# Optimization experiments

Hardware: AMD Instinct MI355X
Metric: run time of the kernel (lower is better)

Reference implementation:

```python
import jax, jax.numpy as jnp
import numpy as np

B, S, IN, IN2, H = 512, 256, 300, 300, 512
FN = 3  # filter_num


def setup_inputs() -> dict:
    key = jax.random.key(0)
    ks = jax.random.split(key, 16)
    def n(k, shape, scale=0.05):
        return jax.random.normal(k, shape, dtype=jnp.float32) * scale
    return {
        "x": jax.random.normal(ks[0], (B, S, IN), dtype=jnp.float32),
        "W_in": n(ks[1], (IN, IN2)), "b_in": n(ks[2], (IN2,)),
        "Wih": n(ks[3], (IN2, 4 * H)), "Whh": n(ks[4], (H, 4 * H)),
        "bih": n(ks[5], (4 * H,)), "bhh": n(ks[6], (4 * H,)),
        "Q": n(ks[7], (H, IN2)), "R": n(ks[8], (IN2, H)),
        "Wc3": n(ks[9], (FN, 1, 3, H)), "bc3": n(ks[10], (FN,)),
        "Wc4": n(ks[11], (FN, 1, 4, H)), "bc4": n(ks[12], (FN,)),
        "Wc5": n(ks[13], (FN, 1, 5, H)), "bc5": n(ks[14], (FN,)),
        "W_lin": n(ks[15], (3 * FN, 2)), "b_lin": jnp.zeros((2,), jnp.float32),
    }


def reference(x, W_in, b_in, Wih, Whh, bih, bhh, Q, R,
              Wc3, bc3, Wc4, bc4, Wc5, bc5, W_lin, b_lin):
    # input projection: [B,S,IN] -> [B,S,IN2]
    xin = jnp.tanh(x @ W_in + b_in)
    xs = jnp.swapaxes(xin, 0, 1)  # [S,B,IN2] for scan
    bsz = x.shape[0]
    h0 = jnp.zeros((bsz, H), x.dtype)
    c0 = jnp.zeros((bsz, H), x.dtype)

    def step(carry, xt):
        ht, Ct = carry
        # mogrify, mog_iterations=2: i=1 odd updates x, i=2 even updates h
        xt = 2.0 * jax.nn.sigmoid(ht @ Q) * xt
        ht = 2.0 * jax.nn.sigmoid(xt @ R) * ht
        gates = xt @ Wih + bih + ht @ Whh + bhh  # [B,4H]
        i, f, g, o = jnp.split(gates, 4, axis=1)
        Ct = jax.nn.sigmoid(f) * Ct + jax.nn.sigmoid(i) * jnp.tanh(g)
        ht = jax.nn.sigmoid(o) * jnp.tanh(Ct)
        return (ht, Ct), ht

    _, hs = jax.lax.scan(step, (h0, c0), xs)  # [S,B,H]
    hmap = jnp.swapaxes(hs, 0, 1)[:, None, :, :]  # [B,1,S,H]

    feats = []
    for w, b in ((Wc3, bc3), (Wc4, bc4), (Wc5, bc5)):
        y = jax.lax.conv_general_dilated(
            hmap, w, (1, 1), 'VALID',
            dimension_numbers=('NCHW', 'OIHW', 'NCHW'))
        y = jax.nn.relu(y + b[None, :, None, None])  # [B,FN,S-fsz+1,1]
        feats.append(jnp.max(y, axis=(2, 3)))  # global max pool -> [B,FN]
    cat = jnp.concatenate(feats, axis=1)  # [B, 3*FN]
    # dropout is identity at inference
    return cat @ W_lin + b_lin  # [B,2]
```

## Files before the change

kernel.cpp:

```cpp
#include <hip/hip_runtime.h>

#define DI __device__ __forceinline__

typedef __attribute__((ext_vector_type(4))) float  f32x4;
typedef __attribute__((ext_vector_type(8))) short  s16x8;
typedef __attribute__((ext_vector_type(8))) __bf16 bf16x8;
typedef unsigned long long u64;

constexpr int S_   = 256;
constexpr int B_   = 512;
constexpr int KP_  = 320;
constexpr int ALD_ = 832;
constexpr int NRING = 34;
constexpr int NWG  = 512;
constexpr size_t HSLOT = 512 * 512;

constexpr size_t OFF_XIN = 0;
constexpr size_t SZ_XIN  = (size_t)S_ * B_ * KP_ * 2;
constexpr size_t OFF_U   = OFF_XIN + SZ_XIN;
constexpr size_t SZ_U    = (size_t)B_ * S_ * 64 * 4;
constexpr size_t OFF_HS  = OFF_U + SZ_U;
constexpr size_t SZ_HS   = (size_t)NRING * HSLOT * 2;
constexpr size_t OFF_ACT = OFF_HS + SZ_HS;
constexpr size_t SZ_ACT  = (size_t)B_ * ALD_ * 2;
constexpr size_t OFF_WPT = OFF_ACT + SZ_ACT;
constexpr size_t SZ_WPT  = (size_t)320 * 320 * 2;
constexpr size_t OFF_QPT = OFF_WPT + SZ_WPT;
constexpr size_t SZ_QPT  = (size_t)320 * 512 * 2;
constexpr size_t OFF_RPT = OFF_QPT + SZ_QPT;
constexpr size_t SZ_RPT  = (size_t)512 * 320 * 2;
constexpr size_t OFF_WGT = OFF_RPT + SZ_RPT;
constexpr size_t SZ_WGT  = (size_t)2048 * 832 * 2;
constexpr size_t OFF_BG  = OFF_WGT + SZ_WGT;
constexpr size_t SZ_BG   = 2048 * 4;
constexpr size_t OFF_VT  = OFF_BG + SZ_BG;
constexpr size_t SZ_VT   = (size_t)64 * 512 * 2;
constexpr size_t OFF_BAR = OFF_VT + SZ_VT;
constexpr size_t SZ_BAR  = 8192;
constexpr size_t WS_NEED = OFF_BAR + SZ_BAR;

DI unsigned short f2bf(float x) {
  unsigned int u = __float_as_uint(x);
  unsigned int r = (u + 0x7FFFu + ((u >> 16) & 1u)) >> 16;
  return (unsigned short)r;
}
DI float bf2f(unsigned short h) { return __uint_as_float(((unsigned int)h) << 16); }

DI float sigm(float x) {
  float e = __builtin_amdgcn_exp2f(x * -1.44269504088896f);
  return __builtin_amdgcn_rcpf(1.0f + e);
}
DI float tanh_(float x) {
  x = fminf(fmaxf(x, -15.0f), 15.0f);
  float e = __builtin_amdgcn_exp2f(x * 2.88539008177793f);
  return (e - 1.0f) * __builtin_amdgcn_rcpf(e + 1.0f);
}
DI bf16x8 asbf(s16x8 v) { return __builtin_bit_cast(bf16x8, v); }

DI u64 ld_sys_u64(const void* p) {
  return __hip_atomic_load((const u64*)p, __ATOMIC_RELAXED, __HIP_MEMORY_SCOPE_SYSTEM);
}
DI void st_sys_u64(void* p, u64 v) {
  __hip_atomic_store((u64*)p, v, __ATOMIC_RELAXED, __HIP_MEMORY_SCOPE_SYSTEM);
}
template<int N> DI void wait_vm() {
  asm volatile("s_waitcnt vmcnt(%0)" :: "n"(N) : "memory");
}

template<int NK>
DI void gemm2(const unsigned short* Ab, int lda,
              const unsigned short* Bb, int ldb,
              short* sA, short* sB, f32x4 acc[2])
{
  constexpr int NR = (NK + 1) / 2;
  const int tid  = threadIdx.x;
  const int tm   = tid >> 8;
  const int t8   = tid & 255;
  const int lane = tid & 63;
  const int l15  = lane & 15;
  const int kseg = (lane >> 4) * 8;
  const int w    = (tid >> 6) & 3;
  const int wm = w >> 1, wn = w & 1;
  const int sArow = t8 >> 3, sAcol = (t8 & 7) * 4;
  const int sBrow = t8 >> 2, sBcol = (t8 & 3) * 8;
  const unsigned short* gA = Ab + sArow * lda + sAcol;
  const unsigned short* gB = Bb + sBrow * ldb + sBcol;
  short* tA = sA + tm * 2048;
  short* tB = sB + tm * 4096;
  const int aoff = sArow * 32 + sAcol;
  const int boff = sBrow * 32 + sBcol;
  const int afr  = (wm * 16 + l15) * 32 + kseg;

  u64 a0, a1 = 0, b00, b01, b10 = 0, b11 = 0;
  a0  = ld_sys_u64(gA + tm * 32);
  b00 = ((const u64*)(gB + tm * 32))[0];
  b01 = ((const u64*)(gB + tm * 32))[1];
  if (2 + tm < NK) {
    a1  = ld_sys_u64(gA + (2 + tm) * 32);
    b10 = ((const u64*)(gB + (2 + tm) * 32))[0];
    b11 = ((const u64*)(gB + (2 + tm) * 32))[1];
  }
  *(u64*)&tA[aoff] = a0;
  *(u64*)&tB[boff] = b00; *(u64*)&tB[boff + 4] = b01;
  __syncthreads();
  #pragma unroll
  for (int j = 0; j < NR; ++j) {
    const int curA = (j & 1) * 1024, curB = (j & 1) * 2048;
    if (j + 2 < NR) {
      const int kt = (j + 2) * 2 + tm;
      if (kt < NK) {
        if ((j & 1) == 0) { a0 = ld_sys_u64(gA + kt * 32);
                            b00 = ((const u64*)(gB + kt * 32))[0];
                            b01 = ((const u64*)(gB + kt * 32))[1]; }
        else              { a1 = ld_sys_u64(gA + kt * 32);
                            b10 = ((const u64*)(gB + kt * 32))[0];
                            b11 = ((const u64*)(gB + kt * 32))[1]; }
      }
    }
    if (j * 2 + tm < NK) {
      s16x8 Af = *(const s16x8*)&tA[curA + afr];
      #pragma unroll
      for (int ni = 0; ni < 2; ++ni) {
        s16x8 Bf = *(const s16x8*)&tB[curB + (wn * 32 + ni * 16 + l15) * 32 + kseg];
        acc[ni] = __builtin_amdgcn_mfma_f32_16x16x32_bf16(asbf(Af), asbf(Bf), acc[ni], 0, 0, 0);
      }
    }
    if (j + 1 < NR) {
      const int kt = (j + 1) * 2 + tm;
      const int nxtA = ((j + 1) & 1) * 1024, nxtB = ((j + 1) & 1) * 2048;
      if (kt < NK) {
        if ((j & 1) == 0) { *(u64*)&tA[nxtA + aoff] = a1;
                            *(u64*)&tB[nxtB + boff] = b10; *(u64*)&tB[nxtB + boff + 4] = b11; }
        else              { *(u64*)&tA[nxtA + aoff] = a0;
                            *(u64*)&tB[nxtB + boff] = b00; *(u64*)&tB[nxtB + boff + 4] = b01; }
      }
    }
    __syncthreads();
  }
}

DI void reduce2(f32x4 acc[2], float* rbuf) {
  const int tid = threadIdx.x, t8 = tid & 255;
  if (tid >= 256) {
    #pragma unroll
    for (int ni = 0; ni < 2; ++ni)
      #pragma unroll
      for (int r = 0; r < 4; ++r)
        rbuf[(ni * 4 + r) * 256 + t8] = acc[ni][r];
  }
  __syncthreads();
  if (tid < 256) {
    #pragma unroll
    for (int ni = 0; ni < 2; ++ni)
      #pragma unroll
      for (int r = 0; r < 4; ++r)
        acc[ni][r] += rbuf[(ni * 4 + r) * 256 + t8];
  }
}

template<typename F>
DI void epiloop32(f32x4 acc[2], F&& f) {
  const int lane = threadIdx.x & 63;
  const int w = (threadIdx.x >> 6) & 3, wm = w >> 1, wn = w & 1;
  #pragma unroll
  for (int ni = 0; ni < 2; ++ni)
    #pragma unroll
    for (int r = 0; r < 4; ++r)
      f(wm * 16 + (lane >> 4) * 4 + r, wn * 32 + ni * 16 + (lane & 15), acc[ni][r]);
}

DI void pack_store32(const unsigned short* lds16, unsigned short* dstbase, int ldd) {
  const u64* l64 = (const u64*)lds16;
  const int i = threadIdx.x;
  const int row = i >> 4, q = i & 15;
  st_sys_u64(dstbase + row * ldd + q * 4, l64[i]);
}

template<int NK, int KREAL>
DI void gemm_f32A(const float* Af, int lda,
                  const unsigned short* Bb, int ldb,
                  short* sA, short* sB, f32x4 acc[2][2])
{
  const int tid  = threadIdx.x;
  const int lane = tid & 63;
  const int w = tid >> 6, wm = w >> 1, wn = w & 1;
  const float* ga = Af + (tid >> 2) * lda;
  const int cseg  = (tid & 3) * 8;
  const unsigned short* gb = Bb + (tid >> 2) * ldb + (tid & 3) * 8;
  const int arow0 = (wm * 32 + (lane & 15)) * 32 + (lane >> 4) * 8;
  const int brow0 = (wn * 32 + (lane & 15)) * 32 + (lane >> 4) * 8;

  auto loadA = [&](int k) -> s16x8 {
    s16x8 r;
    const int c0 = k * 32 + cseg;
    if (c0 + 8 <= KREAL) {
      float4 f0 = *(const float4*)(ga + c0);
      float4 f1 = *(const float4*)(ga + c0 + 4);
      r[0] = (short)f2bf(f0.x); r[1] = (short)f2bf(f0.y);
      r[2] = (short)f2bf(f0.z); r[3] = (short)f2bf(f0.w);
      r[4] = (short)f2bf(f1.x); r[5] = (short)f2bf(f1.y);
      r[6] = (short)f2bf(f1.z); r[7] = (short)f2bf(f1.w);
    } else {
      #pragma unroll
      for (int j = 0; j < 8; ++j) {
        float x = (c0 + j < KREAL) ? ga[c0 + j] : 0.0f;
        r[j] = (short)f2bf(x);
      }
    }
    return r;
  };

  s16x8 va = loadA(0);
  s16x8 vb = *(const s16x8*)gb;
  *(s16x8*)&sA[tid * 8] = va;
  *(s16x8*)&sB[tid * 8] = vb;
  __syncthreads();
  for (int k = 0; k < NK; ++k) {
    const int cur = (k & 1) * 2048;
    if (k + 1 < NK) {
      va = loadA(k + 1);
      vb = *(const s16x8*)(gb + (k + 1) * 32);
    }
    s16x8 a0 = *(const s16x8*)&sA[cur + arow0];
    s16x8 a1 = *(const s16x8*)&sA[cur + arow0 + 16 * 32];
    s16x8 b0 = *(const s16x8*)&sB[cur + brow0];
    s16x8 b1 = *(const s16x8*)&sB[cur + brow0 + 16 * 32];
    acc[0][0] = __builtin_amdgcn_mfma_f32_16x16x32_bf16(asbf(a0), asbf(b0), acc[0][0], 0, 0, 0);
    acc[0][1] = __builtin_amdgcn_mfma_f32_16x16x32_bf16(asbf(a0), asbf(b1), acc[0][1], 0, 0, 0);
    acc[1][0] = __builtin_amdgcn_mfma_f32_16x16x32_bf16(asbf(a1), asbf(b0), acc[1][0], 0, 0, 0);
    acc[1][1] = __builtin_amdgcn_mfma_f32_16x16x32_bf16(asbf(a1), asbf(b1), acc[1][1], 0, 0, 0);
    if (k + 1 < NK) {
      const int nxt = ((k + 1) & 1) * 2048;
      *(s16x8*)&sA[nxt + tid * 8] = va;
      *(s16x8*)&sB[nxt + tid * 8] = vb;
    }
    __syncthreads();
  }
}

template<typename F>
DI void epiloop(f32x4 acc[2][2], F&& f) {
  const int lane = threadIdx.x & 63;
  const int w = (threadIdx.x & 255) >> 6, wm = w >> 1, wn = w & 1;
  #pragma unroll
  for (int mi = 0; mi < 2; ++mi)
    #pragma unroll
    for (int ni = 0; ni < 2; ++ni)
      #pragma unroll
      for (int r = 0; r < 4; ++r) {
        const int rowl = wm * 32 + mi * 16 + (lane >> 4) * 4 + r;
        const int coll = wn * 32 + ni * 16 + (lane & 15);
        f(rowl, coll, acc[mi][ni][r]);
      }
}

__global__ void k_prep_wpt(const float* __restrict__ Wi, unsigned short* __restrict__ WpT) {
  int i = blockIdx.x * 256 + threadIdx.x;
  if (i >= 320 * 320) return;
  int n = i / 320, k = i % 320;
  float v = (n < 300 && k < 300) ? Wi[k * 300 + n] : 0.0f;
  WpT[i] = f2bf(v);
}
__global__ void k_prep_qpt(const float* __restrict__ Q, unsigned short* __restrict__ QpT) {
  int i = blockIdx.x * 256 + threadIdx.x;
  if (i >= 320 * 512) return;
  int n = i >> 9, k = i & 511;
  float v = (n < 300) ? Q[k * 300 + n] : 0.0f;
  QpT[i] = f2bf(v);
}
__global__ void k_prep_rpt(const float* __restrict__ R, unsigned short* __restrict__ RpT) {
  int i = blockIdx.x * 256 + threadIdx.x;
  if (i >= 512 * 320) return;
  int n = i / 320, k = i % 320;
  float v = (k < 300) ? R[k * 512 + n] : 0.0f;
  RpT[i] = f2bf(v);
}
__global__ void k_prep_wgt(const float* __restrict__ Wih, const float* __restrict__ Whh,
                           unsigned short* __restrict__ WgT) {
  int i = blockIdx.x * 256 + threadIdx.x;
  if (i >= 2048 * 832) return;
  int np = i / 832, k = i % 832;
  int c = np >> 2, g = np & 3, col = g * 512 + c;
  float v = 0.0f;
  if (k < 300) v = Wih[k * 2048 + col];
  else if (k >= 320) v = Whh[(k - 320) * 2048 + col];
  WgT[i] = f2bf(v);
}
__global__ void k_prep_bg(const float* __restrict__ bih, const float* __restrict__ bhh,
                          float* __restrict__ bg) {
  int i = blockIdx.x * 256 + threadIdx.x;
  if (i >= 2048) return;
  int c = i >> 2, g = i & 3, col = g * 512 + c;
  bg[i] = bih[col] + bhh[col];
}
__global__ void k_prep_vt(const float* __restrict__ Wc3, const float* __restrict__ Wc4,
                          const float* __restrict__ Wc5, unsigned short* __restrict__ VT) {
  int i = blockIdx.x * 256 + threadIdx.x;
  if (i >= 64 * 512) return;
  int j = i >> 9, k = i & 511;
  float v = 0.0f;
  if (j < 9)       { int f = j / 3,  dt = j % 3;        v = Wc3[(f * 3 + dt) * 512 + k]; }
  else if (j < 21) { int jj = j - 9;  int f = jj / 4, dt = jj % 4; v = Wc4[(f * 4 + dt) * 512 + k]; }
  else if (j < 36) { int jj = j - 21; int f = jj / 5, dt = jj % 5; v = Wc5[(f * 5 + dt) * 512 + k]; }
  VT[i] = f2bf(v);
}
__global__ void k_wsfail(float* out, int n, float v) {
  int i = blockIdx.x * 256 + threadIdx.x;
  if (i < n) out[i] = -v;
}

__global__ __launch_bounds__(256) void k_proj(const float* __restrict__ x,
                                              const unsigned short* __restrict__ WpT,
                                              const float* __restrict__ b_in,
                                              unsigned short* __restrict__ xin) {
  __shared__ short sA[4096], sB[4096];
  const int m0 = blockIdx.x * 64, n0 = blockIdx.y * 64;
  f32x4 acc[2][2];
  const f32x4 z = {0.f, 0.f, 0.f, 0.f};
  acc[0][0] = z; acc[0][1] = z; acc[1][0] = z; acc[1][1] = z;
  gemm_f32A<10, 300>(x + (size_t)m0 * 300, 300, WpT + n0 * 320, 320, sA, sB, acc);
  epiloop(acc, [&](int rowl, int coll, float vacc) {
    const int row = m0 + rowl, col = n0 + coll;
    float o = 0.0f;
    if (col < 300) o = tanh_(vacc + b_in[col]);
    const int b = row >> 8, s = row & 255;
    xin[(size_t)(s * 512 + b) * KP_ + col] = f2bf(o);
  });
}

__global__ __launch_bounds__(512, 4) void k_scan(
    const unsigned short* __restrict__ xin,
    const unsigned short* __restrict__ QpT,
    const unsigned short* __restrict__ RpT,
    const unsigned short* __restrict__ WgT,
    const float* __restrict__ bg,
    const unsigned short* __restrict__ VT,
    unsigned short* __restrict__ hs,
    unsigned short* __restrict__ act,
    float* __restrict__ U,
    unsigned int* __restrict__ bar)
{
  __shared__ short sA[4096];
  __shared__ short sB[8192];
  __shared__ float rbuf[2048];
  __shared__ float gbuf[2048];
  __shared__ unsigned short pbuf[2048];
  __shared__ unsigned short obuf[2048];
  const int wg   = blockIdx.x;
  const int grp  = wg >> 5;
  const int l    = wg & 31;
  const int tid  = threadIdx.x;
  const f32x4 z = {0.f, 0.f, 0.f, 0.f};

  const int gm0 = grp * 32;
  const int gn0 = l * 64;
  float c_state = 0.f;
  const int crow = tid >> 4, ccl = tid & 15;
  const float4 cb = *(const float4*)&bg[gn0 + ccl * 4];

  int ep = 0;
  auto bar_sync = [&]() {
    wait_vm<0>();
    __syncthreads();
    if (tid == 0) {
      __hip_atomic_fetch_add(&bar[grp * 64], 1u,
                             __ATOMIC_RELAXED, __HIP_MEMORY_SCOPE_AGENT);
      const unsigned tgt = (unsigned)(ep + 1) * 32u;
      while (__hip_atomic_load(&bar[grp * 64], __ATOMIC_RELAXED,
                               __HIP_MEMORY_SCOPE_AGENT) < tgt)
        __builtin_amdgcn_s_sleep(1);
    }
    __syncthreads();
    ++ep;
  };

  for (int t = 0; t < S_; ++t) {
    const unsigned short* hst = hs + (size_t)(t % NRING) * HSLOT;
    unsigned short*       hso = hs + (size_t)((t + 1) % NRING) * HSLOT;

    if (l < 5) {
      const int n0 = l * 64;
      {
        const unsigned short* xin_t = xin + ((size_t)t * 512 + gm0) * KP_;
        const int row = tid >> 4, q = tid & 15;
        ((u64*)pbuf)[tid] = *(const u64*)(xin_t + row * KP_ + n0 + q * 4);
      }
      f32x4 acc[2] = {z, z};
      gemm2<16>(hst + gm0 * 512, 512, QpT + n0 * 512, 512, sA, sB, acc);
      reduce2(acc, rbuf);
      if (tid < 256) {
        epiloop32(acc, [&](int row, int col, float v) {
          obuf[row * 64 + col] = f2bf(2.0f * sigm(v) * bf2f(pbuf[row * 64 + col]));
        });
      }
      __syncthreads();
      pack_store32(obuf, act + gm0 * ALD_ + n0, ALD_);
    }
    bar_sync();

    if (l < 8) {
      const int n0 = l * 64;
      {
        const int row = tid >> 4, q = tid & 15;
        ((u64*)pbuf)[tid] = ld_sys_u64(hst + (gm0 + row) * 512 + n0 + q * 4);
      }
      f32x4 acc[2] = {z, z};
      gemm2<10>(act + gm0 * ALD_, ALD_, RpT + n0 * KP_, KP_, sA, sB, acc);
      reduce2(acc, rbuf);
      if (tid < 256) {
        epiloop32(acc, [&](int row, int col, float v) {
          obuf[row * 64 + col] = f2bf(2.0f * sigm(v) * bf2f(pbuf[row * 64 + col]));
        });
      }
      __syncthreads();
      pack_store32(obuf, act + gm0 * ALD_ + 320 + n0, ALD_);
    }
    bar_sync();

    {
      f32x4 acc[2] = {z, z};
      gemm2<26>(act + gm0 * ALD_, ALD_, WgT + gn0 * 832, 832, sA, sB, acc);
      reduce2(acc, rbuf);
      if (tid < 256) {
        epiloop32(acc, [&](int row, int col, float v) {
          gbuf[row * 64 + col] = v;
        });
      }
      __syncthreads();
      {
        const float iv = gbuf[crow * 64 + ccl * 4 + 0] + cb.x;
        const float fv = gbuf[crow * 64 + ccl * 4 + 1] + cb.y;
        const float gv = gbuf[crow * 64 + ccl * 4 + 2] + cb.z;
        const float ov = gbuf[crow * 64 + ccl * 4 + 3] + cb.w;
        const float cn = sigm(fv) * c_state + sigm(iv) * tanh_(gv);
        const float h  = sigm(ov) * tanh_(cn);
        c_state = cn;
        obuf[crow * 16 + ccl] = f2bf(h);
      }
      __syncthreads();
      if (tid < 128) {
        const u64* h64 = (const u64*)obuf;
        const int row = tid >> 2, q = tid & 3;
        st_sys_u64(hso + (gm0 + row) * 512 + l * 16 + q * 4, h64[row * 4 + q]);
      }
    }
    bar_sync();

    if ((t & 31) == 31) {
      const int c = t >> 5;
      const int tglob = 32 * c + l;
      const int slot = (tglob + 1) % NRING;
      f32x4 acc[2] = {z, z};
      gemm2<16>(hs + (size_t)slot * HSLOT + (size_t)gm0 * 512, 512, VT, 512, sA, sB, acc);
      reduce2(acc, rbuf);
      if (tid < 256) {
        epiloop32(acc, [&](int row, int col, float v) {
          U[((size_t)(gm0 + row) * 256 + tglob) * 64 + col] = v;
        });
      }
      __syncthreads();
    }
  }
}

__global__ __launch_bounds__(256) void k_combine(const float* __restrict__ U,
                                                 const float* __restrict__ bc3,
                                                 const float* __restrict__ bc4,
                                                 const float* __restrict__ bc5,
                                                 const float* __restrict__ Wl,
                                                 const float* __restrict__ bl,
                                                 float* __restrict__ out) {
  const int b = blockIdx.x;
  const int p = threadIdx.x;
  const float* Ub = U + (size_t)b * (256 * 64);
  float v[9];
  #pragma unroll
  for (int j = 0; j < 9; ++j) v[j] = -1e30f;
  if (p < 254) {
    #pragma unroll
    for (int f = 0; f < 3; ++f)
      v[f] = Ub[(p + 0) * 64 + f * 3 + 0] + Ub[(p + 1) * 64 + f * 3 + 1] + Ub[(p + 2) * 64 + f * 3 + 2];
  }
  if (p < 253) {
    #pragma unroll
    for (int f = 0; f < 3; ++f)
      v[3 + f] = Ub[(p + 0) * 64 + 9 + f * 4 + 0] + Ub[(p + 1) * 64 + 9 + f * 4 + 1] +
                 Ub[(p + 2) * 64 + 9 + f * 4 + 2] + Ub[(p + 3) * 64 + 9 + f * 4 + 3];
  }
  if (p < 252) {
    #pragma unroll
    for (int f = 0; f < 3; ++f)
      v[6 + f] = Ub[(p + 0) * 64 + 21 + f * 5 + 0] + Ub[(p + 1) * 64 + 21 + f * 5 + 1] +
                 Ub[(p + 2) * 64 + 21 + f * 5 + 2] + Ub[(p + 3) * 64 + 21 + f * 5 + 3] +
                 Ub[(p + 4) * 64 + 21 + f * 5 + 4];
  }
  __shared__ float red[4][9];
  const int lane = threadIdx.x & 63, w = threadIdx.x >> 6;
  #pragma unroll
  for (int j = 0; j < 9; ++j) {
    float m = v[j];
    #pragma unroll
    for (int off = 32; off >= 1; off >>= 1) m = fmaxf(m, __shfl_xor(m, off));
    if (lane == 0) red[w][j] = m;
  }
  __syncthreads();
  if (threadIdx.x < 2) {
    const int k = threadIdx.x;
    float o = bl[k];
    #pragma unroll
    for (int j = 0; j < 9; ++j) {
      float m = fmaxf(fmaxf(red[0][j], red[1][j]), fmaxf(red[2][j], red[3][j]));
      float bias = (j < 3) ? bc3[j] : (j < 6) ? bc4[j - 3] : bc5[j - 6];
      o += fmaxf(m + bias, 0.0f) * Wl[j * 2 + k];
    }
    out[b * 2 + k] = o;
  }
}

extern "C" void kernel_launch(void* const* d_in, const int* in_sizes, int n_in,
                              void* d_out, int out_size, void* d_ws, size_t ws_size,
                              hipStream_t stream) {
  const float* x     = (const float*)d_in[0];
  const float* W_in  = (const float*)d_in[1];
  const float* b_in  = (const float*)d_in[2];
  const float* Wih   = (const float*)d_in[3];
  const float* Whh   = (const float*)d_in[4];
  const float* bih   = (const float*)d_in[5];
  const float* bhh   = (const float*)d_in[6];
  const float* Q     = (const float*)d_in[7];
  const float* R     = (const float*)d_in[8];
  const float* Wc3   = (const float*)d_in[9];
  const float* bc3   = (const float*)d_in[10];
  const float* Wc4   = (const float*)d_in[11];
  const float* bc4   = (const float*)d_in[12];
  const float* Wc5   = (const float*)d_in[13];
  const float* bc5   = (const float*)d_in[14];
  const float* W_lin = (const float*)d_in[15];
  const float* b_lin = (const float*)d_in[16];

  if (ws_size < WS_NEED) {
    k_wsfail<<<4, 256, 0, stream>>>((float*)d_out, out_size, (float)(ws_size >> 20));
    return;
  }

  char* ws = (char*)d_ws;
  unsigned short* xin = (unsigned short*)(ws + OFF_XIN);
  float*          U   = (float*)(ws + OFF_U);
  unsigned short* hs  = (unsigned short*)(ws + OFF_HS);
  unsigned short* act = (unsigned short*)(ws + OFF_ACT);
  unsigned short* WpT = (unsigned short*)(ws + OFF_WPT);
  unsigned short* QpT = (unsigned short*)(ws + OFF_QPT);
  unsigned short* RpT = (unsigned short*)(ws + OFF_RPT);
  unsigned short* WgT = (unsigned short*)(ws + OFF_WGT);
  float*          bg  = (float*)(ws + OFF_BG);
  unsigned short* VT  = (unsigned short*)(ws + OFF_VT);
  unsigned int*   bar = (unsigned int*)(ws + OFF_BAR);

  (void)hipMemsetAsync(hs, 0, HSLOT * 2, stream);
  (void)hipMemsetAsync(bar, 0, SZ_BAR, stream);

  k_prep_wpt<<<(320 * 320 + 255) / 256, 256, 0, stream>>>(W_in, WpT);
  k_prep_qpt<<<(320 * 512 + 255) / 256, 256, 0, stream>>>(Q, QpT);
  k_prep_rpt<<<(512 * 320 + 255) / 256, 256, 0, stream>>>(R, RpT);
  k_prep_wgt<<<(2048 * 832 + 255) / 256, 256, 0, stream>>>(Wih, Whh, WgT);
  k_prep_bg<<<8, 256, 0, stream>>>(bih, bhh, bg);
  k_prep_vt<<<(64 * 512 + 255) / 256, 256, 0, stream>>>(Wc3, Wc4, Wc5, VT);

  k_proj<<<dim3(131072 / 64, KP_ / 64), 256, 0, stream>>>(x, WpT, b_in, xin);

  k_scan<<<NWG, 512, 0, stream>>>(xin, QpT, RpT, WgT, bg, VT, hs, act, U, bar);

  k_combine<<<512, 256, 0, stream>>>(U, bc3, bc4, bc5, W_lin, b_lin, (float*)d_out);
}
```

Before: 5.543 ms.

## Replace atomic counter barrier with per-workgroup flag barrier and deepen A prefetch

The group barrier changes from a single atomic counter polled by one thread to per-workgroup epoch flags. Each workgroup stores its own flag and a wavefront polls all 32 flags with a vote, which removes the atomic RMW contention and the trailing __syncthreads. The GEMM now prefetches A tiles four stages ahead instead of two, and the x and h operand loads for the mogrifier stages are hoisted to the top of each timestep. The cost is more registers and more reliance on system-scope relaxed ordering, since flags are read by every wave without a fence.

```diff
diff --git a/kernel.cpp b/kernel.cpp
--- a/kernel.cpp
+++ b/kernel.cpp
@@ -63,6 +63,12 @@
 DI void st_sys_u64(void* p, u64 v) {
   __hip_atomic_store((u64*)p, v, __ATOMIC_RELAXED, __HIP_MEMORY_SCOPE_SYSTEM);
 }
+DI unsigned int ld_sys_u32(const unsigned int* p) {
+  return __hip_atomic_load(p, __ATOMIC_RELAXED, __HIP_MEMORY_SCOPE_SYSTEM);
+}
+DI void st_sys_u32(unsigned int* p, unsigned int v) {
+  __hip_atomic_store(p, v, __ATOMIC_RELAXED, __HIP_MEMORY_SCOPE_SYSTEM);
+}
 template<int N> DI void wait_vm() {
   asm volatile("s_waitcnt vmcnt(%0)" :: "n"(N) : "memory");
 }
@@ -91,30 +97,29 @@
   const int boff = sBrow * 32 + sBcol;
   const int afr  = (wm * 16 + l15) * 32 + kseg;
 
-  u64 a0, a1 = 0, b00, b01, b10 = 0, b11 = 0;
-  a0  = ld_sys_u64(gA + tm * 32);
-  b00 = ((const u64*)(gB + tm * 32))[0];
-  b01 = ((const u64*)(gB + tm * 32))[1];
-  if (2 + tm < NK) {
-    a1  = ld_sys_u64(gA + (2 + tm) * 32);
-    b10 = ((const u64*)(gB + (2 + tm) * 32))[0];
-    b11 = ((const u64*)(gB + (2 + tm) * 32))[1];
-  }
-  *(u64*)&tA[aoff] = a0;
-  *(u64*)&tB[boff] = b00; *(u64*)&tB[boff + 4] = b01;
+  u64 a[4] = {}, b0[2] = {}, b1[2] = {};
+  #pragma unroll
+  for (int r = 0; r < 4; ++r)
+    if (r < NR && r * 2 + tm < NK) a[r] = ld_sys_u64(gA + (r * 2 + tm) * 32);
+  #pragma unroll
+  for (int r = 0; r < 2; ++r)
+    if (r < NR && r * 2 + tm < NK) {
+      b0[r] = ((const u64*)(gB + (r * 2 + tm) * 32))[0];
+      b1[r] = ((const u64*)(gB + (r * 2 + tm) * 32))[1];
+    }
+  *(u64*)&tA[aoff] = a[0];
+  *(u64*)&tB[boff] = b0[0]; *(u64*)&tB[boff + 4] = b1[0];
   __syncthreads();
   #pragma unroll
   for (int j = 0; j < NR; ++j) {
     const int curA = (j & 1) * 1024, curB = (j & 1) * 2048;
-    if (j + 2 < NR) {
-      const int kt = (j + 2) * 2 + tm;
-      if (kt < NK) {
-        if ((j & 1) == 0) { a0 = ld_sys_u64(gA + kt * 32);
-                            b00 = ((const u64*)(gB + kt * 32))[0];
-                            b01 = ((const u64*)(gB + kt * 32))[1]; }
-        else              { a1 = ld_sys_u64(gA + kt * 32);
-                            b10 = ((const u64*)(gB + kt * 32))[0];
-                            b11 = ((const u64*)(gB + kt * 32))[1]; }
+    {
+      const int ka = (j + 4) * 2 + tm;
+      if (j + 4 < NR && ka < NK) a[j & 3] = ld_sys_u64(gA + ka * 32);
+      const int kb = (j + 2) * 2 + tm;
+      if (j + 2 < NR && kb < NK) {
+        b0[j & 1] = ((const u64*)(gB + kb * 32))[0];
+        b1[j & 1] = ((const u64*)(gB + kb * 32))[1];
       }
     }
     if (j * 2 + tm < NK) {
@@ -129,10 +134,9 @@
       const int kt = (j + 1) * 2 + tm;
       const int nxtA = ((j + 1) & 1) * 1024, nxtB = ((j + 1) & 1) * 2048;
       if (kt < NK) {
-        if ((j & 1) == 0) { *(u64*)&tA[nxtA + aoff] = a1;
-                            *(u64*)&tB[nxtB + boff] = b10; *(u64*)&tB[nxtB + boff + 4] = b11; }
-        else              { *(u64*)&tA[nxtA + aoff] = a0;
-                            *(u64*)&tB[nxtB + boff] = b00; *(u64*)&tB[nxtB + boff + 4] = b01; }
+        *(u64*)&tA[nxtA + aoff] = a[(j + 1) & 3];
+        *(u64*)&tB[nxtB + boff] = b0[(j + 1) & 1];
+        *(u64*)&tB[nxtB + boff + 4] = b1[(j + 1) & 1];
       }
     }
     __syncthreads();
@@ -350,6 +354,7 @@
   const int grp  = wg >> 5;
   const int l    = wg & 31;
   const int tid  = threadIdx.x;
+  const int lane = tid & 63;
   const f32x4 z = {0.f, 0.f, 0.f, 0.f};
 
   const int gm0 = grp * 32;
@@ -358,19 +363,15 @@
   const int crow = tid >> 4, ccl = tid & 15;
   const float4 cb = *(const float4*)&bg[gn0 + ccl * 4];
 
+  unsigned int* flags = bar + grp * 32;
   int ep = 0;
   auto bar_sync = [&]() {
     wait_vm<0>();
     __syncthreads();
-    if (tid == 0) {
-      __hip_atomic_fetch_add(&bar[grp * 64], 1u,
-                             __ATOMIC_RELAXED, __HIP_MEMORY_SCOPE_AGENT);
-      const unsigned tgt = (unsigned)(ep + 1) * 32u;
-      while (__hip_atomic_load(&bar[grp * 64], __ATOMIC_RELAXED,
-                               __HIP_MEMORY_SCOPE_AGENT) < tgt)
-        __builtin_amdgcn_s_sleep(1);
-    }
-    __syncthreads();
+    const unsigned tag = (unsigned)(ep + 1);
+    if (tid == 0) st_sys_u32(&flags[l], tag);
+    while (!__all(ld_sys_u32(&flags[lane & 31]) >= tag))
+      __builtin_amdgcn_s_sleep(1);
     ++ep;
   };
 
@@ -378,13 +379,16 @@
     const unsigned short* hst = hs + (size_t)(t % NRING) * HSLOT;
     unsigned short*       hso = hs + (size_t)((t + 1) % NRING) * HSLOT;
 
+    u64 xpre = 0, hpre = 0;
+    const int prow = tid >> 4, pq = tid & 15;
+    if (l < 5)
+      xpre = *(const u64*)(xin + ((size_t)t * 512 + gm0 + prow) * KP_ + l * 64 + pq * 4);
+    if (l < 8)
+      hpre = ld_sys_u64(hst + (gm0 + prow) * 512 + l * 64 + pq * 4);
+
     if (l < 5) {
       const int n0 = l * 64;
-      {
-        const unsigned short* xin_t = xin + ((size_t)t * 512 + gm0) * KP_;
-        const int row = tid >> 4, q = tid & 15;
-        ((u64*)pbuf)[tid] = *(const u64*)(xin_t + row * KP_ + n0 + q * 4);
-      }
+      ((u64*)pbuf)[tid] = xpre;
       f32x4 acc[2] = {z, z};
       gemm2<16>(hst + gm0 * 512, 512, QpT + n0 * 512, 512, sA, sB, acc);
       reduce2(acc, rbuf);
@@ -400,10 +404,7 @@
 
     if (l < 8) {
       const int n0 = l * 64;
-      {
-        const int row = tid >> 4, q = tid & 15;
-        ((u64*)pbuf)[tid] = ld_sys_u64(hst + (gm0 + row) * 512 + n0 + q * 4);
-      }
+      ((u64*)pbuf)[tid] = hpre;
       f32x4 acc[2] = {z, z};
       gemm2<10>(act + gm0 * ALD_, ALD_, RpT + n0 * KP_, KP_, sA, sB, acc);
       reduce2(acc, rbuf);
```

Measured after the change: 6.137 ms. 10.7% more time.

## Split gate GEMM and replace second barrier with per-producer flags

Applied to the files above, without the earlier changes.

The gate GEMM is split into the x-part (K=320) and the h-part (K=512). The x-part now starts right after the phase-1 barrier, and only the h-part waits on per-workgroup completion flags published by the 8 producer workgroups of phase 2, replacing a full 32-workgroup group barrier. The x and h prefetch loads are also hoisted to the top of the timestep so their latency overlaps earlier work. This adds flag polling, and correctness now relies on relaxed system-scope stores and loads for ordering the act data.

```diff
diff --git a/kernel.cpp b/kernel.cpp
--- a/kernel.cpp
+++ b/kernel.cpp
@@ -63,6 +63,12 @@
 DI void st_sys_u64(void* p, u64 v) {
   __hip_atomic_store((u64*)p, v, __ATOMIC_RELAXED, __HIP_MEMORY_SCOPE_SYSTEM);
 }
+DI unsigned int ld_sys_u32(const unsigned int* p) {
+  return __hip_atomic_load(p, __ATOMIC_RELAXED, __HIP_MEMORY_SCOPE_SYSTEM);
+}
+DI void st_sys_u32(unsigned int* p, unsigned int v) {
+  __hip_atomic_store(p, v, __ATOMIC_RELAXED, __HIP_MEMORY_SCOPE_SYSTEM);
+}
 template<int N> DI void wait_vm() {
   asm volatile("s_waitcnt vmcnt(%0)" :: "n"(N) : "memory");
 }
@@ -358,16 +364,16 @@
   const int crow = tid >> 4, ccl = tid & 15;
   const float4 cb = *(const float4*)&bg[gn0 + ccl * 4];
 
+  unsigned int* cnt  = bar + grp * 64;
+  unsigned int* p2f  = bar + grp * 64 + 32;
   int ep = 0;
   auto bar_sync = [&]() {
     wait_vm<0>();
     __syncthreads();
     if (tid == 0) {
-      __hip_atomic_fetch_add(&bar[grp * 64], 1u,
-                             __ATOMIC_RELAXED, __HIP_MEMORY_SCOPE_AGENT);
+      __hip_atomic_fetch_add(cnt, 1u, __ATOMIC_RELAXED, __HIP_MEMORY_SCOPE_AGENT);
       const unsigned tgt = (unsigned)(ep + 1) * 32u;
-      while (__hip_atomic_load(&bar[grp * 64], __ATOMIC_RELAXED,
-                               __HIP_MEMORY_SCOPE_AGENT) < tgt)
+      while (__hip_atomic_load(cnt, __ATOMIC_RELAXED, __HIP_MEMORY_SCOPE_AGENT) < tgt)
         __builtin_amdgcn_s_sleep(1);
     }
     __syncthreads();
@@ -378,13 +384,16 @@
     const unsigned short* hst = hs + (size_t)(t % NRING) * HSLOT;
     unsigned short*       hso = hs + (size_t)((t + 1) % NRING) * HSLOT;
 
+    u64 xpre = 0, hpre = 0;
+    const int prow = tid >> 4, pq = tid & 15;
+    if (l < 5)
+      xpre = *(const u64*)(xin + ((size_t)t * 512 + gm0 + prow) * KP_ + l * 64 + pq * 4);
+    if (l < 8)
+      hpre = ld_sys_u64(hst + (gm0 + prow) * 512 + l * 64 + pq * 4);
+
     if (l < 5) {
       const int n0 = l * 64;
-      {
-        const unsigned short* xin_t = xin + ((size_t)t * 512 + gm0) * KP_;
-        const int row = tid >> 4, q = tid & 15;
-        ((u64*)pbuf)[tid] = *(const u64*)(xin_t + row * KP_ + n0 + q * 4);
-      }
+      ((u64*)pbuf)[tid] = xpre;
       f32x4 acc[2] = {z, z};
       gemm2<16>(hst + gm0 * 512, 512, QpT + n0 * 512, 512, sA, sB, acc);
       reduce2(acc, rbuf);
@@ -400,10 +409,7 @@
 
     if (l < 8) {
       const int n0 = l * 64;
-      {
-        const int row = tid >> 4, q = tid & 15;
-        ((u64*)pbuf)[tid] = ld_sys_u64(hst + (gm0 + row) * 512 + n0 + q * 4);
-      }
+      ((u64*)pbuf)[tid] = hpre;
       f32x4 acc[2] = {z, z};
       gemm2<10>(act + gm0 * ALD_, ALD_, RpT + n0 * KP_, KP_, sA, sB, acc);
       reduce2(acc, rbuf);
@@ -414,12 +420,25 @@
       }
       __syncthreads();
       pack_store32(obuf, act + gm0 * ALD_ + 320 + n0, ALD_);
-    }
-    bar_sync();
+      wait_vm<0>();
+      __syncthreads();
+      if (tid == 0) st_sys_u32(&p2f[l], (unsigned)(t + 1));
+    }
+
+    f32x4 acc[2] = {z, z};
+    gemm2<10>(act + gm0 * ALD_, ALD_, WgT + gn0 * 832, 832, sA, sB, acc);
 
     {
-      f32x4 acc[2] = {z, z};
-      gemm2<26>(act + gm0 * ALD_, ALD_, WgT + gn0 * 832, 832, sA, sB, acc);
+      const unsigned tag = (unsigned)(t + 1);
+      if (tid < 64) {
+        while (!__all(ld_sys_u32(&p2f[tid & 7]) >= tag))
+          __builtin_amdgcn_s_sleep(1);
+      }
+      __syncthreads();
+    }
+
+    {
+      gemm2<16>(act + gm0 * ALD_ + 320, ALD_, WgT + gn0 * 832 + 320, 832, sA, sB, acc);
       reduce2(acc, rbuf);
       if (tid < 256) {
         epiloop32(acc, [&](int row, int col, float v) {
@@ -450,11 +469,11 @@
       const int c = t >> 5;
       const int tglob = 32 * c + l;
       const int slot = (tglob + 1) % NRING;
-      f32x4 acc[2] = {z, z};
-      gemm2<16>(hs + (size_t)slot * HSLOT + (size_t)gm0 * 512, 512, VT, 512, sA, sB, acc);
-      reduce2(acc, rbuf);
+      f32x4 acu[2] = {z, z};
+      gemm2<16>(hs + (size_t)slot * HSLOT + (size_t)gm0 * 512, 512, VT, 512, sA, sB, acu);
+      reduce2(acu, rbuf);
       if (tid < 256) {
-        epiloop32(acc, [&](int row, int col, float v) {
+        epiloop32(acu, [&](int row, int col, float v) {
           U[((size_t)(gm0 + row) * 256 + tglob) * 64 + col] = v;
         });
       }
```

Measured after the change: 5.357 ms (median of 2 runs). 1.03x faster.
